# Kernel tuning notes

Hardware: AMD Instinct MI355X
Metric: run time of the kernel (lower is better)

The kernel has to match this reference:

```python
import jax, jax.numpy as jnp
import numpy as np

N = 50000      # nodes
E = 1000000    # edges
NF = 5         # node_features
EF = 2         # edge_features
RS = 128       # rnn_size
RES = 32       # rnn_edge_size
H = 4          # heads
C = 16         # out_features
FIN = RS + RES # GAT in_channels
NEG_SLOPE = 0.2


def lstm_step(x, h, c, Wih, Whh, bih, bhh):
    # Single-step LSTM (torch gate order: i, f, g, o)
    g = x @ Wih.T + h @ Whh.T + bih + bhh
    i, f, gg, o = jnp.split(g, 4, axis=-1)
    i = jax.nn.sigmoid(i); f = jax.nn.sigmoid(f)
    gg = jnp.tanh(gg); o = jax.nn.sigmoid(o)
    c2 = f * c + i * gg
    return o * jnp.tanh(c2), c2


def setup_inputs() -> dict:
    key = jax.random.key(0)
    ks = jax.random.split(key, 20)
    p = lambda k, shape: (jax.random.normal(k, shape) * 0.1).astype(jnp.float32)
    return dict(
        x=jax.random.normal(ks[0], (N, NF), jnp.float32),
        edge_index=jax.random.randint(ks[1], (2, E), 0, N),
        edge_attr=jax.random.normal(ks[2], (E, EF), jnp.float32),
        h_node_h=p(ks[3], (N, RS)), h_node_c=p(ks[4], (N, RS)),
        h_edge_h=p(ks[5], (E, RES)), h_edge_c=p(ks[6], (E, RES)),
        Wih_n=p(ks[7], (4 * RS, NF)), Whh_n=p(ks[8], (4 * RS, RS)),
        bih_n=p(ks[9], (4 * RS,)), bhh_n=p(ks[10], (4 * RS,)),
        Wih_e=p(ks[11], (4 * RES, EF)), Whh_e=p(ks[12], (4 * RES, RES)),
        bih_e=p(ks[13], (4 * RES,)), bhh_e=p(ks[14], (4 * RES,)),
        W_gat=p(ks[15], (FIN, H * C)),
        att_src=p(ks[16], (H, C)), att_dst=p(ks[17], (H, C)),
        bias_gat=p(ks[18], (C,)),
    )


def reference(x, edge_index, edge_attr, h_node_h, h_node_c, h_edge_h, h_edge_c,
              Wih_n, Whh_n, bih_n, bhh_n, Wih_e, Whh_e, bih_e, bhh_e,
              W_gat, att_src, att_dst, bias_gat):
    n = x.shape[0]
    # --- edge history encoder: per-edge LSTM step + scatter-mean to dst nodes ---
    he, ce = lstm_step(edge_attr, h_edge_h, h_edge_c, Wih_e, Whh_e, bih_e, bhh_e)
    dst0 = edge_index[1]
    esum = jax.ops.segment_sum(he, dst0, num_segments=n)
    deg = jax.ops.segment_sum(jnp.ones((he.shape[0], 1), he.dtype), dst0, num_segments=n)
    edge_enc = esum / jnp.maximum(deg, 1.0)            # [N, RES]
    # --- node history encoder: per-node LSTM step ---
    hn, cn = lstm_step(x, h_node_h, h_node_c, Wih_n, Whh_n, bih_n, bhh_n)
    feat = jnp.concatenate([hn, edge_enc], axis=-1)    # [N, FIN]
    # --- GATConv (PyG v1 style, add_self_loops=True, concat=False) ---
    xl = (feat @ W_gat).reshape(n, H, C)               # [N, H, C]
    a_src = jnp.einsum('nhc,hc->nh', xl, att_src)
    a_dst = jnp.einsum('nhc,hc->nh', xl, att_dst)
    loops = jnp.arange(n)
    src = jnp.concatenate([edge_index[0], loops])
    dst = jnp.concatenate([edge_index[1], loops])
    alpha = jax.nn.leaky_relu(a_src[src] + a_dst[dst], NEG_SLOPE)  # [E+N, H]
    m = jax.ops.segment_max(alpha, dst, num_segments=n)
    ea = jnp.exp(alpha - m[dst])
    s = jax.ops.segment_sum(ea, dst, num_segments=n)
    w = ea / s[dst]                                     # segment softmax over dst
    out = jax.ops.segment_sum(xl[src] * w[:, :, None], dst, num_segments=n)  # [N,H,C]
    out = out.mean(axis=1) + bias_gat                   # concat=False -> head mean
    return (out, hn, cn, he, ce)
```

## Files before the change

### kernel.cpp

```cpp
#include <hip/hip_runtime.h>

#define CAP 128

typedef __attribute__((ext_vector_type(8))) short bf16x8;
typedef __attribute__((ext_vector_type(4))) float f32x4;

__device__ __forceinline__ float sigf(float x) {
    return __builtin_amdgcn_rcpf(1.0f + __expf(-x));
}
__device__ __forceinline__ float tanhfast(float x) {
    return 2.0f * __builtin_amdgcn_rcpf(1.0f + __expf(-2.0f * x)) - 1.0f;
}
__device__ __forceinline__ short bfr(float f) {
    unsigned u = __float_as_uint(f);
    unsigned r = (u + 0x7FFFu + ((u >> 16) & 1u)) >> 16;
    return (short)r;
}
__device__ __forceinline__ bf16x8 cvt8(const float* p) {
    const float4* q = (const float4*)p;
    float4 u = q[0], v = q[1];
    bf16x8 r;
    r[0]=bfr(u.x); r[1]=bfr(u.y); r[2]=bfr(u.z); r[3]=bfr(u.w);
    r[4]=bfr(v.x); r[5]=bfr(v.y); r[6]=bfr(v.z); r[7]=bfr(v.w);
    return r;
}

__global__ void convert_kernel(
    const float* __restrict__ Whh_n, const float* __restrict__ Wih_n,
    const float* __restrict__ bih_n, const float* __restrict__ bhh_n,
    const float* __restrict__ Whh_e, const float* __restrict__ Wih_e,
    const float* __restrict__ bih_e, const float* __restrict__ bhh_e,
    const float* __restrict__ Wgat,
    unsigned short* __restrict__ WnF, unsigned short* __restrict__ WeF,
    unsigned short* __restrict__ WgF, float* __restrict__ bsn, float* __restrict__ bse)
{
    int i = blockIdx.x * 256 + threadIdx.x;
    if (i < 512 * 160) {
        int j = i & 7, unit = i >> 3;
        int lane = unit & 63, tk = unit >> 6;
        int t = tk / 5, k4 = tk - t * 5;
        int r = t * 16 + (lane & 15);
        int k = k4 * 32 + (lane >> 4) * 8 + j;
        float v = (k < 128) ? Whh_n[r * 128 + k] : (k < 133 ? Wih_n[r * 5 + (k - 128)] : 0.f);
        WnF[i] = (unsigned short)bfr(v);
    }
    if (i < 128 * 64) {
        int j = i & 7, unit = i >> 3;
        int lane = unit & 63, ts = unit >> 6;
        int t = ts >> 1, s = ts & 1;
        int r = t * 16 + (lane & 15);
        int k = s * 32 + (lane >> 4) * 8 + j;
        float v = (k < 32) ? Whh_e[r * 32 + k] : (k < 34 ? Wih_e[r * 2 + (k - 32)] : 0.f);
        WeF[i] = (unsigned short)bfr(v);
    }
    if (i < 64 * 160) {
        int j = i & 7, unit = i >> 3;
        int lane = unit & 63, tk = unit >> 6;
        int t = tk / 5, k4 = tk - t * 5;
        int r = t * 16 + (lane & 15);
        int k = k4 * 32 + (lane >> 4) * 8 + j;
        WgF[i] = (unsigned short)bfr(Wgat[k * 64 + r]);
    }
    if (i < 512) bsn[i] = bih_n[i] + bhh_n[i];
    if (i < 128) bse[i] = bih_e[i] + bhh_e[i];
}

__global__ void csr_fill_kernel(const int* __restrict__ dst, int* __restrict__ cnt,
                                int* __restrict__ eid, int E)
{
    int e = blockIdx.x * blockDim.x + threadIdx.x;
    if (e >= E) return;
    int d = dst[e];
    int k = atomicAdd(cnt + d, 1);
    if (k < CAP) eid[(size_t)d * CAP + k] = e;
}

__global__ __launch_bounds__(256) void edge_lstm_mfma(
    const float* __restrict__ eattr, const float* __restrict__ h_in, const float* __restrict__ c_in,
    const unsigned short* __restrict__ WeF, const float* __restrict__ bse,
    float* __restrict__ he_out, float* __restrict__ ce_out, int E)
{
    const int lane = threadIdx.x & 63, wave = threadIdx.x >> 6;
    const int lr = lane & 15, lg = lane >> 4;
    const bf16x8* Wv = (const bf16x8*)WeF;
    bf16x8 wa0[8], wa1[8];
    #pragma unroll
    for (int t = 0; t < 8; ++t) {
        wa0[t] = Wv[(t * 2 + 0) * 64 + lane];
        wa1[t] = Wv[(t * 2 + 1) * 64 + lane];
    }
    const int jb0 = lg * 4, jb1 = 16 + lg * 4;
    const f32x4 bi0 = *(const f32x4*)(bse + jb0),       bi1 = *(const f32x4*)(bse + jb1);
    const f32x4 bf0 = *(const f32x4*)(bse + 32 + jb0),  bf1 = *(const f32x4*)(bse + 32 + jb1);
    const f32x4 bg0 = *(const f32x4*)(bse + 64 + jb0),  bg1 = *(const f32x4*)(bse + 64 + jb1);
    const f32x4 bo0 = *(const f32x4*)(bse + 96 + jb0),  bo1 = *(const f32x4*)(bse + 96 + jb1);
    const int base = blockIdx.x * 256 + wave * 64;
    #pragma unroll
    for (int tile = 0; tile < 4; ++tile) {
        const int e0 = base + tile * 16;
        if (e0 >= E) break;
        const int edge = e0 + lr;
        bf16x8 b0 = cvt8(h_in + (size_t)edge * 32 + lg * 8);
        bf16x8 b1 = {0,0,0,0,0,0,0,0};
        if (lg == 0) {
            b1[0] = bfr(eattr[(size_t)edge * 2]);
            b1[1] = bfr(eattr[(size_t)edge * 2 + 1]);
        }
        f32x4 acc[8];
        #pragma unroll
        for (int t = 0; t < 8; ++t) {
            f32x4 v = {0, 0, 0, 0};
            v = __builtin_amdgcn_mfma_f32_16x16x32_bf16(wa0[t], b0, v, 0, 0, 0);
            v = __builtin_amdgcn_mfma_f32_16x16x32_bf16(wa1[t], b1, v, 0, 0, 0);
            acc[t] = v;
        }
        #pragma unroll
        for (int u = 0; u < 2; ++u) {
            const int jb = u * 16 + lg * 4;
            const f32x4 bi = u ? bi1 : bi0, bf_ = u ? bf1 : bf0;
            const f32x4 bg_ = u ? bg1 : bg0, bo_ = u ? bo1 : bo0;
            f32x4 cold = *(const f32x4*)(c_in + (size_t)edge * 32 + jb);
            f32x4 cres, hres;
            #pragma unroll
            for (int q = 0; q < 4; ++q) {
                float gi = acc[u][q] + bi[q],      gf = acc[u + 2][q] + bf_[q];
                float gg = acc[u + 4][q] + bg_[q], go = acc[u + 6][q] + bo_[q];
                float c2 = sigf(gf) * cold[q] + sigf(gi) * tanhfast(gg);
                cres[q] = c2;
                hres[q] = sigf(go) * tanhfast(c2);
            }
            __builtin_nontemporal_store(cres, (f32x4*)(ce_out + (size_t)edge * 32 + jb));
            *(f32x4*)(he_out + (size_t)edge * 32 + jb) = hres;
        }
    }
}

__global__ __launch_bounds__(256) void node_lstm_mfma(
    const float* __restrict__ x, const float* __restrict__ h_in, const float* __restrict__ c_in,
    const unsigned short* __restrict__ WnF, const float* __restrict__ bsn,
    float* __restrict__ hn_out, float* __restrict__ cn_out, int N)
{
    const int lane = threadIdx.x & 63, wave = threadIdx.x >> 6;
    const int n0 = blockIdx.x * 64 + wave * 16;
    if (n0 >= N) return;
    const int lr = lane & 15, lg = lane >> 4;
    const int node = n0 + lr;
    bf16x8 b[5];
    const float* hp = h_in + (size_t)node * 128 + lg * 8;
    b[0] = cvt8(hp); b[1] = cvt8(hp + 32); b[2] = cvt8(hp + 64); b[3] = cvt8(hp + 96);
    bf16x8 bx = {0,0,0,0,0,0,0,0};
    if (lg == 0) {
        const float* xp = x + (size_t)node * 5;
        bx[0]=bfr(xp[0]); bx[1]=bfr(xp[1]); bx[2]=bfr(xp[2]); bx[3]=bfr(xp[3]); bx[4]=bfr(xp[4]);
    }
    b[4] = bx;
    const bf16x8* Wv = (const bf16x8*)WnF;
    f32x4 acc[32];
    #pragma unroll
    for (int t = 0; t < 32; ++t) {
        const bf16x8* ap = Wv + t * 320 + lane;
        f32x4 v = {0, 0, 0, 0};
        #pragma unroll
        for (int k4 = 0; k4 < 5; ++k4)
            v = __builtin_amdgcn_mfma_f32_16x16x32_bf16(ap[k4 * 64], b[k4], v, 0, 0, 0);
        acc[t] = v;
    }
    #pragma unroll
    for (int u = 0; u < 8; ++u) {
        const int jb = u * 16 + lg * 4;
        f32x4 bi  = *(const f32x4*)(bsn + jb);
        f32x4 bf_ = *(const f32x4*)(bsn + 128 + jb);
        f32x4 bg_ = *(const f32x4*)(bsn + 256 + jb);
        f32x4 bo_ = *(const f32x4*)(bsn + 384 + jb);
        f32x4 cold = *(const f32x4*)(c_in + (size_t)node * 128 + jb);
        f32x4 cres, hres;
        #pragma unroll
        for (int q = 0; q < 4; ++q) {
            float gi = acc[u][q] + bi[q],       gf = acc[u + 8][q] + bf_[q];
            float gg = acc[u + 16][q] + bg_[q], go = acc[u + 24][q] + bo_[q];
            float c2 = sigf(gf) * cold[q] + sigf(gi) * tanhfast(gg);
            cres[q] = c2;
            hres[q] = sigf(go) * tanhfast(c2);
        }
        __builtin_nontemporal_store(cres, (f32x4*)(cn_out + (size_t)node * 128 + jb));
        *(f32x4*)(hn_out + (size_t)node * 128 + jb) = hres;
    }
}

__global__ __launch_bounds__(256) void edge_enc_kernel(
    const int* __restrict__ cnt, const int* __restrict__ eid,
    const float* __restrict__ he, float* __restrict__ enc, int N)
{
    const int wid = (blockIdx.x * blockDim.x + threadIdx.x) >> 6;
    const int lane = threadIdx.x & 63;
    if (wid >= N) return;
    const int c = cnt[wid];
    const int m = min(c, CAP);
    const int g = lane >> 3, l8 = lane & 7;
    const int* el = eid + (size_t)wid * CAP;
    f32x4 acc = {0, 0, 0, 0};
    for (int i = g; i < m; i += 8)
        acc += *(const f32x4*)(he + (size_t)el[i] * 32 + l8 * 4);
    #pragma unroll
    for (int off = 8; off < 64; off <<= 1) {
        acc[0] += __shfl_xor(acc[0], off);
        acc[1] += __shfl_xor(acc[1], off);
        acc[2] += __shfl_xor(acc[2], off);
        acc[3] += __shfl_xor(acc[3], off);
    }
    if (g == 0) {
        float inv = 1.0f / fmaxf((float)c, 1.0f);
        f32x4 r; r[0]=acc[0]*inv; r[1]=acc[1]*inv; r[2]=acc[2]*inv; r[3]=acc[3]*inv;
        *(f32x4*)(enc + (size_t)wid * 32 + l8 * 4) = r;
    }
}

__global__ __launch_bounds__(256) void gat_xl_mfma(
    const float* __restrict__ hn, const float* __restrict__ enc,
    const unsigned short* __restrict__ WgF,
    const float* __restrict__ attS, const float* __restrict__ attD,
    float* __restrict__ xl, float* __restrict__ asrc, float* __restrict__ adst, int N)
{
    const int lane = threadIdx.x & 63, wave = threadIdx.x >> 6;
    const int n0 = blockIdx.x * 64 + wave * 16;
    if (n0 >= N) return;
    const int lr = lane & 15, lg = lane >> 4;
    const int node = n0 + lr;
    bf16x8 b[5];
    const float* hp = hn + (size_t)node * 128 + lg * 8;
    b[0] = cvt8(hp); b[1] = cvt8(hp + 32); b[2] = cvt8(hp + 64); b[3] = cvt8(hp + 96);
    b[4] = cvt8(enc + (size_t)node * 32 + lg * 8);
    const bf16x8* Wv = (const bf16x8*)WgF;
    #pragma unroll
    for (int t = 0; t < 4; ++t) {
        const bf16x8* ap = Wv + t * 320 + lane;
        f32x4 v = {0, 0, 0, 0};
        #pragma unroll
        for (int k4 = 0; k4 < 5; ++k4)
            v = __builtin_amdgcn_mfma_f32_16x16x32_bf16(ap[k4 * 64], b[k4], v, 0, 0, 0);
        *(f32x4*)(xl + (size_t)node * 64 + t * 16 + lg * 4) = v;
        const f32x4 ws = *(const f32x4*)(attS + t * 16 + lg * 4);
        const f32x4 wd = *(const f32x4*)(attD + t * 16 + lg * 4);
        float p1 = v[0]*ws[0] + v[1]*ws[1] + v[2]*ws[2] + v[3]*ws[3];
        float p2 = v[0]*wd[0] + v[1]*wd[1] + v[2]*wd[2] + v[3]*wd[3];
        p1 += __shfl_xor(p1, 16); p2 += __shfl_xor(p2, 16);
        p1 += __shfl_xor(p1, 32); p2 += __shfl_xor(p2, 32);
        if (lg == 0) {
            asrc[(size_t)node * 4 + t] = p1;
            adst[(size_t)node * 4 + t] = p2;
        }
    }
}

__global__ __launch_bounds__(256) void gat_node_kernel(
    const int* __restrict__ cnt, const int* __restrict__ eid,
    const int* __restrict__ src_idx,
    const float* __restrict__ asrc, const float* __restrict__ adst,
    const float* __restrict__ xl, const float* __restrict__ bias,
    float* __restrict__ out, int N)
{
    const int wid = (blockIdx.x * blockDim.x + threadIdx.x) >> 6;
    const int lane = threadIdx.x & 63;
    if (wid >= N) return;
    const int n = wid;
    const int m = min(cnt[n], CAP);
    const int h = lane >> 4, c16 = lane & 15;
    const int nslot = (m + 15) >> 4;
    const float ad = adst[n * 4 + h];
    float aself = asrc[n * 4 + h] + ad;
    aself = aself > 0.f ? aself : 0.2f * aself;
    const int* el = eid + (size_t)n * CAP;
    int   ss[8];
    float aa[8];
    float mx = aself;
    #pragma unroll
    for (int k = 0; k < 8; ++k) {
        if (k >= nslot) break;
        int i = k * 16 + c16;
        if (i < m) {
            int s = src_idx[el[i]];
            float a = asrc[s * 4 + h] + ad;
            a = a > 0.f ? a : 0.2f * a;
            ss[k] = s; aa[k] = a;
            mx = fmaxf(mx, a);
        } else { ss[k] = 0; aa[k] = -1e30f; }
    }
    #pragma unroll
    for (int off = 1; off < 16; off <<= 1) mx = fmaxf(mx, __shfl_xor(mx, off));
    float ea[8];
    float p = 0.f;
    #pragma unroll
    for (int k = 0; k < 8; ++k) {
        if (k >= nslot) break;
        ea[k] = __expf(aa[k] - mx);
        p += ea[k];
    }
    #pragma unroll
    for (int off = 1; off < 16; off <<= 1) p += __shfl_xor(p, off);
    float eself = __expf(aself - mx);
    float sacc = eself + p;
    float oacc = eself * xl[(size_t)n * 64 + lane];
    const int grp = lane & 48;
    #pragma unroll
    for (int k = 0; k < 8; ++k) {
        if (k >= nslot) break;
        const int lim = min(16, m - k * 16);
        #pragma unroll 4
        for (int cc = 0; cc < lim; ++cc) {
            int srcl = grp | cc;
            float w = __shfl(ea[k], srcl);
            int   s = __shfl(ss[k], srcl);
            oacc += w * xl[(size_t)s * 64 + lane];
        }
    }
    float r = oacc / sacc;
    r += __shfl_xor(r, 16);
    r += __shfl_xor(r, 32);
    if (lane < 16) out[(size_t)n * 16 + lane] = 0.25f * r + bias[lane];
}

extern "C" void kernel_launch(void* const* d_in, const int* in_sizes, int n_in,
                              void* d_out, int out_size, void* d_ws, size_t ws_size,
                              hipStream_t stream)
{
    const float* x     = (const float*)d_in[0];
    const int*   ei    = (const int*)  d_in[1];
    const float* eattr = (const float*)d_in[2];
    const float* hn_h  = (const float*)d_in[3];
    const float* hn_c  = (const float*)d_in[4];
    const float* he_h  = (const float*)d_in[5];
    const float* he_c  = (const float*)d_in[6];
    const float* Wih_n = (const float*)d_in[7];
    const float* Whh_n = (const float*)d_in[8];
    const float* bih_n = (const float*)d_in[9];
    const float* bhh_n = (const float*)d_in[10];
    const float* Wih_e = (const float*)d_in[11];
    const float* Whh_e = (const float*)d_in[12];
    const float* bih_e = (const float*)d_in[13];
    const float* bhh_e = (const float*)d_in[14];
    const float* W_gat = (const float*)d_in[15];
    const float* attS  = (const float*)d_in[16];
    const float* attD  = (const float*)d_in[17];
    const float* biasG = (const float*)d_in[18];

    const int N = in_sizes[0] / 5;
    const int E = in_sizes[2] / 2;

    float* out = (float*)d_out;
    float* hn  = out + (size_t)N * 16;
    float* cn  = hn  + (size_t)N * 128;
    float* he  = cn  + (size_t)N * 128;
    float* ce  = he  + (size_t)E * 32;

    char* p = (char*)d_ws;
    size_t off = 0;
    auto take = [&](size_t bytes) -> void* {
        void* r = p + off;
        off = (off + bytes + 255) & ~(size_t)255;
        return r;
    };
    int*   cnt  = (int*)  take((size_t)N * 4);
    int*   eid  = (int*)  take((size_t)N * CAP * 4);
    float* enc  = (float*)take((size_t)N * 32 * 4);
    float* xl   = (float*)take((size_t)N * 64 * 4);
    float* asrc = (float*)take((size_t)N * 4 * 4);
    float* adst = (float*)take((size_t)N * 4 * 4);
    unsigned short* WnF = (unsigned short*)take(512 * 160 * 2);
    unsigned short* WeF = (unsigned short*)take(128 * 64 * 2);
    unsigned short* WgF = (unsigned short*)take(64 * 160 * 2);
    float* bsn = (float*)take(512 * 4);
    float* bse = (float*)take(128 * 4);

    hipMemsetAsync(cnt, 0, (size_t)N * 4, stream);
    convert_kernel<<<(512 * 160 + 255) / 256, 256, 0, stream>>>(
        Whh_n, Wih_n, bih_n, bhh_n, Whh_e, Wih_e, bih_e, bhh_e, W_gat,
        WnF, WeF, WgF, bsn, bse);
    csr_fill_kernel<<<(E + 255) / 256, 256, 0, stream>>>(ei + E, cnt, eid, E);
    edge_lstm_mfma<<<(E + 255) / 256, 256, 0, stream>>>(
        eattr, he_h, he_c, WeF, bse, he, ce, E);
    node_lstm_mfma<<<(N + 63) / 64, 256, 0, stream>>>(
        x, hn_h, hn_c, WnF, bsn, hn, cn, N);
    edge_enc_kernel<<<(N + 3) / 4, 256, 0, stream>>>(cnt, eid, he, enc, N);
    gat_xl_mfma<<<(N + 63) / 64, 256, 0, stream>>>(
        hn, enc, WgF, attS, attD, xl, asrc, adst, N);
    gat_node_kernel<<<(N + 3) / 4, 256, 0, stream>>>(
        cnt, eid, ei, asrc, adst, xl, biasG, out, N);
}
```

Measured before the change: 388.3 us.

## Fuse CSR fill, edge encoder and GAT projection; store xl in bf16

The counter memset moves into the weight-conversion kernel. The CSR bucket fill moves into the edge LSTM kernel, and the edge-encoder scatter-mean is merged into the GAT projection kernel, passing through shared memory instead of a global enc buffer. The xl projection is stored as bf16, which halves the traffic of the per-edge gathers in the attention aggregation. In exchange there are fewer launches and less intermediate global traffic, but the fused encoder walks 16 nodes serially per wave with far fewer waves in flight, and the bf16 xl adds rounding error.

```diff
diff --git a/kernel.cpp b/kernel.cpp
--- a/kernel.cpp
+++ b/kernel.cpp
@@ -15,6 +15,9 @@
     unsigned u = __float_as_uint(f);
     unsigned r = (u + 0x7FFFu + ((u >> 16) & 1u)) >> 16;
     return (short)r;
+}
+__device__ __forceinline__ float bf2f(unsigned short u) {
+    return __uint_as_float(((unsigned)u) << 16);
 }
 __device__ __forceinline__ bf16x8 cvt8(const float* p) {
     const float4* q = (const float4*)p;
@@ -32,9 +35,11 @@
     const float* __restrict__ bih_e, const float* __restrict__ bhh_e,
     const float* __restrict__ Wgat,
     unsigned short* __restrict__ WnF, unsigned short* __restrict__ WeF,
-    unsigned short* __restrict__ WgF, float* __restrict__ bsn, float* __restrict__ bse)
+    unsigned short* __restrict__ WgF, float* __restrict__ bsn, float* __restrict__ bse,
+    int* __restrict__ cnt, int N)
 {
     int i = blockIdx.x * 256 + threadIdx.x;
+    if (i < N) cnt[i] = 0;
     if (i < 512 * 160) {
         int j = i & 7, unit = i >> 3;
         int lane = unit & 63, tk = unit >> 6;
@@ -65,22 +70,22 @@
     if (i < 128) bse[i] = bih_e[i] + bhh_e[i];
 }
 
-__global__ void csr_fill_kernel(const int* __restrict__ dst, int* __restrict__ cnt,
-                                int* __restrict__ eid, int E)
-{
-    int e = blockIdx.x * blockDim.x + threadIdx.x;
-    if (e >= E) return;
-    int d = dst[e];
-    int k = atomicAdd(cnt + d, 1);
-    if (k < CAP) eid[(size_t)d * CAP + k] = e;
-}
-
 __global__ __launch_bounds__(256) void edge_lstm_mfma(
     const float* __restrict__ eattr, const float* __restrict__ h_in, const float* __restrict__ c_in,
     const unsigned short* __restrict__ WeF, const float* __restrict__ bse,
+    const int* __restrict__ dst, int* __restrict__ cnt, int* __restrict__ eid,
     float* __restrict__ he_out, float* __restrict__ ce_out, int E)
 {
     const int lane = threadIdx.x & 63, wave = threadIdx.x >> 6;
+    const int base = blockIdx.x * 256 + wave * 64;
+    {
+        const int edge = base + lane;
+        if (edge < E) {
+            int d = dst[edge];
+            int k = atomicAdd(cnt + d, 1);
+            if (k < CAP) eid[(size_t)d * CAP + k] = edge;
+        }
+    }
     const int lr = lane & 15, lg = lane >> 4;
     const bf16x8* Wv = (const bf16x8*)WeF;
     bf16x8 wa0[8], wa1[8];
@@ -94,7 +99,6 @@
     const f32x4 bf0 = *(const f32x4*)(bse + 32 + jb0),  bf1 = *(const f32x4*)(bse + 32 + jb1);
     const f32x4 bg0 = *(const f32x4*)(bse + 64 + jb0),  bg1 = *(const f32x4*)(bse + 64 + jb1);
     const f32x4 bo0 = *(const f32x4*)(bse + 96 + jb0),  bo1 = *(const f32x4*)(bse + 96 + jb1);
-    const int base = blockIdx.x * 256 + wave * 64;
     #pragma unroll
     for (int tile = 0; tile < 4; ++tile) {
         const int e0 = base + tile * 16;
@@ -187,49 +191,44 @@
     }
 }
 
-__global__ __launch_bounds__(256) void edge_enc_kernel(
-    const int* __restrict__ cnt, const int* __restrict__ eid,
-    const float* __restrict__ he, float* __restrict__ enc, int N)
-{
-    const int wid = (blockIdx.x * blockDim.x + threadIdx.x) >> 6;
-    const int lane = threadIdx.x & 63;
-    if (wid >= N) return;
-    const int c = cnt[wid];
-    const int m = min(c, CAP);
+__global__ __launch_bounds__(256) void enc_gatxl_kernel(
+    const int* __restrict__ cnt, const int* __restrict__ eid, const float* __restrict__ he,
+    const float* __restrict__ hn, const unsigned short* __restrict__ WgF,
+    const float* __restrict__ attS, const float* __restrict__ attD,
+    unsigned short* __restrict__ xlb, float* __restrict__ asrc, float* __restrict__ adst, int N)
+{
+    __shared__ float encs[64 * 36];
+    const int lane = threadIdx.x & 63, wave = threadIdx.x >> 6;
+    const int nbase = blockIdx.x * 64 + wave * 16;
+    if (nbase >= N) return;
     const int g = lane >> 3, l8 = lane & 7;
-    const int* el = eid + (size_t)wid * CAP;
-    f32x4 acc = {0, 0, 0, 0};
-    for (int i = g; i < m; i += 8)
-        acc += *(const f32x4*)(he + (size_t)el[i] * 32 + l8 * 4);
-    #pragma unroll
-    for (int off = 8; off < 64; off <<= 1) {
-        acc[0] += __shfl_xor(acc[0], off);
-        acc[1] += __shfl_xor(acc[1], off);
-        acc[2] += __shfl_xor(acc[2], off);
-        acc[3] += __shfl_xor(acc[3], off);
-    }
-    if (g == 0) {
-        float inv = 1.0f / fmaxf((float)c, 1.0f);
-        f32x4 r; r[0]=acc[0]*inv; r[1]=acc[1]*inv; r[2]=acc[2]*inv; r[3]=acc[3]*inv;
-        *(f32x4*)(enc + (size_t)wid * 32 + l8 * 4) = r;
-    }
-}
-
-__global__ __launch_bounds__(256) void gat_xl_mfma(
-    const float* __restrict__ hn, const float* __restrict__ enc,
-    const unsigned short* __restrict__ WgF,
-    const float* __restrict__ attS, const float* __restrict__ attD,
-    float* __restrict__ xl, float* __restrict__ asrc, float* __restrict__ adst, int N)
-{
-    const int lane = threadIdx.x & 63, wave = threadIdx.x >> 6;
-    const int n0 = blockIdx.x * 64 + wave * 16;
-    if (n0 >= N) return;
+    for (int t = 0; t < 16; ++t) {
+        const int node = nbase + t;
+        const int c = cnt[node];
+        const int m = min(c, CAP);
+        const int* el = eid + (size_t)node * CAP;
+        f32x4 acc = {0, 0, 0, 0};
+        for (int i = g; i < m; i += 8)
+            acc += *(const f32x4*)(he + (size_t)el[i] * 32 + l8 * 4);
+        #pragma unroll
+        for (int off = 8; off < 64; off <<= 1) {
+            acc[0] += __shfl_xor(acc[0], off);
+            acc[1] += __shfl_xor(acc[1], off);
+            acc[2] += __shfl_xor(acc[2], off);
+            acc[3] += __shfl_xor(acc[3], off);
+        }
+        if (g == 0) {
+            float inv = 1.0f / fmaxf((float)c, 1.0f);
+            f32x4 r; r[0]=acc[0]*inv; r[1]=acc[1]*inv; r[2]=acc[2]*inv; r[3]=acc[3]*inv;
+            *(f32x4*)(&encs[(wave * 16 + t) * 36 + l8 * 4]) = r;
+        }
+    }
     const int lr = lane & 15, lg = lane >> 4;
-    const int node = n0 + lr;
+    const int node = nbase + lr;
     bf16x8 b[5];
     const float* hp = hn + (size_t)node * 128 + lg * 8;
     b[0] = cvt8(hp); b[1] = cvt8(hp + 32); b[2] = cvt8(hp + 64); b[3] = cvt8(hp + 96);
-    b[4] = cvt8(enc + (size_t)node * 32 + lg * 8);
+    b[4] = cvt8(&encs[(wave * 16 + lr) * 36 + lg * 8]);
     const bf16x8* Wv = (const bf16x8*)WgF;
     #pragma unroll
     for (int t = 0; t < 4; ++t) {
@@ -238,7 +237,10 @@
         #pragma unroll
         for (int k4 = 0; k4 < 5; ++k4)
             v = __builtin_amdgcn_mfma_f32_16x16x32_bf16(ap[k4 * 64], b[k4], v, 0, 0, 0);
-        *(f32x4*)(xl + (size_t)node * 64 + t * 16 + lg * 4) = v;
+        ushort4 pk;
+        pk.x = (unsigned short)bfr(v[0]); pk.y = (unsigned short)bfr(v[1]);
+        pk.z = (unsigned short)bfr(v[2]); pk.w = (unsigned short)bfr(v[3]);
+        *(ushort4*)(xlb + (size_t)node * 64 + t * 16 + lg * 4) = pk;
         const f32x4 ws = *(const f32x4*)(attS + t * 16 + lg * 4);
         const f32x4 wd = *(const f32x4*)(attD + t * 16 + lg * 4);
         float p1 = v[0]*ws[0] + v[1]*ws[1] + v[2]*ws[2] + v[3]*ws[3];
@@ -256,7 +258,7 @@
     const int* __restrict__ cnt, const int* __restrict__ eid,
     const int* __restrict__ src_idx,
     const float* __restrict__ asrc, const float* __restrict__ adst,
-    const float* __restrict__ xl, const float* __restrict__ bias,
+    const unsigned short* __restrict__ xlb, const float* __restrict__ bias,
     float* __restrict__ out, int N)
 {
     const int wid = (blockIdx.x * blockDim.x + threadIdx.x) >> 6;
@@ -299,7 +301,7 @@
     for (int off = 1; off < 16; off <<= 1) p += __shfl_xor(p, off);
     float eself = __expf(aself - mx);
     float sacc = eself + p;
-    float oacc = eself * xl[(size_t)n * 64 + lane];
+    float oacc = eself * bf2f(xlb[(size_t)n * 64 + lane]);
     const int grp = lane & 48;
     #pragma unroll
     for (int k = 0; k < 8; ++k) {
@@ -310,7 +312,7 @@
             int srcl = grp | cc;
             float w = __shfl(ea[k], srcl);
             int   s = __shfl(ss[k], srcl);
-            oacc += w * xl[(size_t)s * 64 + lane];
+            oacc += w * bf2f(xlb[(size_t)s * 64 + lane]);
         }
     }
     float r = oacc / sacc;
@@ -361,8 +363,7 @@
     };
     int*   cnt  = (int*)  take((size_t)N * 4);
     int*   eid  = (int*)  take((size_t)N * CAP * 4);
-    float* enc  = (float*)take((size_t)N * 32 * 4);
-    float* xl   = (float*)take((size_t)N * 64 * 4);
+    unsigned short* xlb = (unsigned short*)take((size_t)N * 64 * 2);
     float* asrc = (float*)take((size_t)N * 4 * 4);
     float* adst = (float*)take((size_t)N * 4 * 4);
     unsigned short* WnF = (unsigned short*)take(512 * 160 * 2);
@@ -371,18 +372,15 @@
     float* bsn = (float*)take(512 * 4);
     float* bse = (float*)take(128 * 4);
 
-    hipMemsetAsync(cnt, 0, (size_t)N * 4, stream);
     convert_kernel<<<(512 * 160 + 255) / 256, 256, 0, stream>>>(
         Whh_n, Wih_n, bih_n, bhh_n, Whh_e, Wih_e, bih_e, bhh_e, W_gat,
-        WnF, WeF, WgF, bsn, bse);
-    csr_fill_kernel<<<(E + 255) / 256, 256, 0, stream>>>(ei + E, cnt, eid, E);
+        WnF, WeF, WgF, bsn, bse, cnt, N);
     edge_lstm_mfma<<<(E + 255) / 256, 256, 0, stream>>>(
-        eattr, he_h, he_c, WeF, bse, he, ce, E);
+        eattr, he_h, he_c, WeF, bse, ei + E, cnt, eid, he, ce, E);
     node_lstm_mfma<<<(N + 63) / 64, 256, 0, stream>>>(
         x, hn_h, hn_c, WnF, bsn, hn, cn, N);
-    edge_enc_kernel<<<(N + 3) / 4, 256, 0, stream>>>(cnt, eid, he, enc, N);
-    gat_xl_mfma<<<(N + 63) / 64, 256, 0, stream>>>(
-        hn, enc, WgF, attS, attD, xl, asrc, adst, N);
+    enc_gatxl_kernel<<<(N + 63) / 64, 256, 0, stream>>>(
+        cnt, eid, he, hn, WgF, attS, attD, xlb, asrc, adst, N);
     gat_node_kernel<<<(N + 3) / 4, 256, 0, stream>>>(
-        cnt, eid, ei, asrc, adst, xl, biasG, out, N);
-}
+        cnt, eid, ei, asrc, adst, xlb, biasG, out, N);
+}
```

New measurement: 370.1 us. -4.7%, faster.
